# Kernel tuning notes

Hardware: AMD Instinct MI355X
Metric: run time of the kernel (lower is better)

## Reference

```python
import jax, jax.numpy as jnp
import numpy as np

B, S, IN, D, H, FF, L = 16, 1000, 32, 512, 8, 2048, 6
DK = D // H
EPS = 1e-5


def setup_inputs() -> dict:
    key = jax.random.key(0)
    ks = iter(jax.random.split(key, 64))
    def w(shape, s=0.02):
        return jax.random.normal(next(ks), shape, dtype=jnp.float32) * s
    inp = {
        'x': jax.random.normal(next(ks), (B, S, IN), dtype=jnp.float32),
        # input projection
        'Win': w((IN, D)), 'b_in': jnp.zeros((D,), jnp.float32),
        # per-layer attention weights (stacked over L layers)
        'Wq': w((L, D, D)), 'bq': jnp.zeros((L, D), jnp.float32),
        'Wk': w((L, D, D)), 'bk': jnp.zeros((L, D), jnp.float32),
        'Wv': w((L, D, D)), 'bv': jnp.zeros((L, D), jnp.float32),
        'Wo': w((L, D, D)), 'bo': jnp.zeros((L, D), jnp.float32),
        # per-layer feed-forward
        'W1': w((L, D, FF)), 'b1': jnp.zeros((L, FF), jnp.float32),
        'W2': w((L, FF, D)), 'b2': jnp.zeros((L, D), jnp.float32),
        # per-layer layernorms
        'ln1_g': jnp.ones((L, D), jnp.float32), 'ln1_b': jnp.zeros((L, D), jnp.float32),
        'ln2_g': jnp.ones((L, D), jnp.float32), 'ln2_b': jnp.zeros((L, D), jnp.float32),
        # final encoder norm
        'lnf_g': jnp.ones((D,), jnp.float32), 'lnf_b': jnp.zeros((D,), jnp.float32),
        # feature extraction head: D -> D/2 -> D/4
        'Wf1': w((D, D // 2)), 'bf1': jnp.zeros((D // 2,), jnp.float32),
        'Wf2': w((D // 2, D // 4)), 'bf2': jnp.zeros((D // 4,), jnp.float32),
        # reconstruction head: D/4 -> D/2 -> D -> IN
        'Wr1': w((D // 4, D // 2)), 'br1': jnp.zeros((D // 2,), jnp.float32),
        'Wr2': w((D // 2, D)), 'br2': jnp.zeros((D,), jnp.float32),
        'Wr3': w((D, IN)), 'br3': jnp.zeros((IN,), jnp.float32),
        # anomaly head: D/4 -> D/8 -> 1
        'Wa1': w((D // 4, D // 8)), 'ba1': jnp.zeros((D // 8,), jnp.float32),
        'Wa2': w((D // 8, 1)), 'ba2': jnp.zeros((1,), jnp.float32),
    }
    return inp


def _layernorm(x, g, b):
    m = jnp.mean(x, axis=-1, keepdims=True)
    v = jnp.var(x, axis=-1, keepdims=True)
    return (x - m) * jax.lax.rsqrt(v + EPS) * g + b


def _pos_encoding(seq_len, d_model):
    pos = jnp.arange(seq_len, dtype=jnp.float32)[:, None]
    div = jnp.exp(jnp.arange(0, d_model, 2, dtype=jnp.float32) * (-np.log(10000.0) / d_model))
    pe = jnp.zeros((seq_len, d_model), jnp.float32)
    pe = pe.at[:, 0::2].set(jnp.sin(pos * div))
    pe = pe.at[:, 1::2].set(jnp.cos(pos * div))
    return pe


def _encoder(h, Wq, bq, Wk, bk, Wv, bv, Wo, bo, W1, b1, W2, b2,
             ln1_g, ln1_b, ln2_g, ln2_b, lnf_g, lnf_b):
    h = h + _pos_encoding(h.shape[1], D)[None]
    scale = 1.0 / np.sqrt(DK)
    for i in range(L):
        # multi-head self-attention
        q = (h @ Wq[i] + bq[i]).reshape(B, S, H, DK).transpose(0, 2, 1, 3)
        k = (h @ Wk[i] + bk[i]).reshape(B, S, H, DK).transpose(0, 2, 1, 3)
        v = (h @ Wv[i] + bv[i]).reshape(B, S, H, DK).transpose(0, 2, 1, 3)
        scores = jnp.einsum('bhsd,bhtd->bhst', q, k) * scale  # [B,H,S,S]
        attn = jax.nn.softmax(scores, axis=-1)
        ctx = jnp.einsum('bhst,bhtd->bhsd', attn, v)
        ctx = ctx.transpose(0, 2, 1, 3).reshape(B, S, D)
        attn_out = ctx @ Wo[i] + bo[i]
        h = _layernorm(h + attn_out, ln1_g[i], ln1_b[i])
        # feed-forward
        ff = jax.nn.relu(h @ W1[i] + b1[i]) @ W2[i] + b2[i]
        h = _layernorm(h + ff, ln2_g[i], ln2_b[i])
    return _layernorm(h, lnf_g, lnf_b)


def reference(x, Win, b_in, Wq, bq, Wk, bk, Wv, bv, Wo, bo, W1, b1, W2, b2,
              ln1_g, ln1_b, ln2_g, ln2_b, lnf_g, lnf_b,
              Wf1, bf1, Wf2, bf2, Wr1, br1, Wr2, br2, Wr3, br3,
              Wa1, ba1, Wa2, ba2):
    h = x @ Win + b_in  # [B,S,D]
    h = _encoder(h, Wq, bq, Wk, bk, Wv, bv, Wo, bo, W1, b1, W2, b2,
                 ln1_g, ln1_b, ln2_g, ln2_b, lnf_g, lnf_b)
    feat = jax.nn.relu(h @ Wf1 + bf1) @ Wf2 + bf2  # [B,S,D/4]
    recon = jax.nn.relu(jax.nn.relu(feat @ Wr1 + br1) @ Wr2 + br2) @ Wr3 + br3  # [B,S,IN]
    anomaly = jax.nn.sigmoid(jax.nn.relu(feat @ Wa1 + ba1) @ Wa2 + ba2)  # [B,S,1]
    return recon, anomaly
```

## Files before the change

### kernel.cpp

```cpp
#include <hip/hip_runtime.h>
#include <hip/hip_bf16.h>
#include <math.h>

#define B_  16
#define S_  1000
#define IN_ 32
#define D_  512
#define H_  8
#define FF_ 2048
#define L_  6
#define DK_ 64
#define M_  (B_ * S_)
#define SP_ 1024

typedef __bf16 bf16x8 __attribute__((ext_vector_type(8)));
typedef float  floatx4 __attribute__((ext_vector_type(4)));

#define FLAG_RELU 1
#define FLAG_BF16 2
#define FLAG_QKV  4

#define QSCALE 0.18033688011112042f

__global__ __launch_bounds__(256) void gemm_mfma(
    const __bf16* __restrict__ A, const __bf16* __restrict__ BT,
    const float* __restrict__ bias, void* __restrict__ C,
    int M, int N, int K, int flags)
{
    __shared__ __bf16 Asm[2][128 * 32];
    __shared__ __bf16 Bsm[2][128 * 32];

    int tid  = threadIdx.x;
    int wave = tid >> 6;
    int lane = tid & 63;
    int bm = blockIdx.y * 128;
    int bn = blockIdx.x * 128;
    int wm = (wave & 1) * 64;
    int wn = (wave >> 1) * 64;
    int lm = lane & 15;
    int lq = lane >> 4;

    floatx4 acc[4][4] = {};

    int crow  = tid >> 2;
    int cpart = (tid & 3) * 8;
    const __bf16* ag0 = A + (size_t)(bm + crow) * K + cpart;
    const __bf16* ag1 = A + (size_t)(bm + 64 + crow) * K + cpart;
    int nr0 = bn + crow, nr1 = bn + 64 + crow;
    const __bf16* bg0 = BT + (size_t)nr0 * K + cpart;
    const __bf16* bg1 = BT + (size_t)nr1 * K + cpart;
    bool bv0 = nr0 < N, bv1 = nr1 < N;

    uint4 pa0, pa1, pb0, pb1;
    pa0 = *(const uint4*)ag0;
    pa1 = *(const uint4*)ag1;
    pb0 = bv0 ? *(const uint4*)bg0 : make_uint4(0, 0, 0, 0);
    pb1 = bv1 ? *(const uint4*)bg1 : make_uint4(0, 0, 0, 0);

    for (int k0 = 0, it = 0; k0 < K; k0 += 32, ++it) {
        const int cur = it & 1;
        *(uint4*)&Asm[cur][tid * 8]        = pa0;
        *(uint4*)&Asm[cur][2048 + tid * 8] = pa1;
        *(uint4*)&Bsm[cur][tid * 8]        = pb0;
        *(uint4*)&Bsm[cur][2048 + tid * 8] = pb1;
        __syncthreads();

        if (k0 + 32 < K) {
            pa0 = *(const uint4*)(ag0 + k0 + 32);
            pa1 = *(const uint4*)(ag1 + k0 + 32);
            pb0 = bv0 ? *(const uint4*)(bg0 + k0 + 32) : make_uint4(0, 0, 0, 0);
            pb1 = bv1 ? *(const uint4*)(bg1 + k0 + 32) : make_uint4(0, 0, 0, 0);
        }

        bf16x8 af[4], bf[4];
        #pragma unroll
        for (int i = 0; i < 4; ++i) {
            af[i] = *(const bf16x8*)&Asm[cur][(wm + i * 16 + lm) * 32 + lq * 8];
            bf[i] = *(const bf16x8*)&Bsm[cur][(wn + i * 16 + lm) * 32 + lq * 8];
        }
        #pragma unroll
        for (int i = 0; i < 4; ++i)
            #pragma unroll
            for (int j = 0; j < 4; ++j)
                acc[i][j] = __builtin_amdgcn_mfma_f32_16x16x32_bf16(
                    af[i], bf[j], acc[i][j], 0, 0, 0);
    }

    if (flags & FLAG_QKV) {
        int sec = bn >> 9;
        if (sec < 2) {
            __bf16* dst = (__bf16*)C + (sec ? (size_t)8192000 : 0);
            #pragma unroll
            for (int j = 0; j < 4; ++j) {
                int col = (bn & 511) + wn + j * 16 + lm;
                float bvv = bias[bn + wn + j * 16 + lm];
                #pragma unroll
                for (int i = 0; i < 4; ++i)
                    #pragma unroll
                    for (int r = 0; r < 4; ++r) {
                        int m = bm + wm + i * 16 + lq * 4 + r;
                        dst[(size_t)m * 512 + col] = (__bf16)(acc[i][j][r] + bvv);
                    }
            }
        } else {
            __bf16* vt = (__bf16*)C + (size_t)16384000;
            int bbq[4], s0[4];
            #pragma unroll
            for (int i = 0; i < 4; ++i) {
                int m0 = bm + wm + i * 16 + lq * 4;
                bbq[i] = m0 / 1000;
                s0[i]  = m0 - bbq[i] * 1000;
            }
            #pragma unroll
            for (int j = 0; j < 4; ++j) {
                int col = (bn & 511) + wn + j * 16 + lm;
                float bvv = bias[bn + wn + j * 16 + lm];
                int head = col >> 6, dk = col & 63;
                #pragma unroll
                for (int i = 0; i < 4; ++i) {
                    __bf16 t4[4];
                    #pragma unroll
                    for (int r = 0; r < 4; ++r) t4[r] = (__bf16)(acc[i][j][r] + bvv);
                    *(uint2*)(vt + ((size_t)(bbq[i] * H_ + head) * DK_ + dk) * SP_ + s0[i])
                        = *(uint2*)t4;
                }
            }
        }
        return;
    }

    #pragma unroll
    for (int j = 0; j < 4; ++j) {
        int n = bn + wn + j * 16 + lm;
        if (n >= N) continue;
        float bv = bias[n];
        #pragma unroll
        for (int i = 0; i < 4; ++i) {
            #pragma unroll
            for (int r = 0; r < 4; ++r) {
                int m = bm + wm + i * 16 + lq * 4 + r;
                float v = acc[i][j][r] + bv;
                if (flags & FLAG_RELU) v = fmaxf(v, 0.f);
                if (flags & FLAG_BF16) ((__bf16*)C)[(size_t)m * N + n] = (__bf16)v;
                else                   ((float*)C)[(size_t)m * N + n] = v;
            }
        }
    }
}

__device__ __forceinline__ void trans_tile(
    const float* __restrict__ src, __bf16* __restrict__ dst,
    int K, int N, float scale, int tx0, int ty0)
{
    __shared__ float t[32][33];
    int n0 = tx0 * 32, k0 = ty0 * 32;
    int tx = threadIdx.x & 31, ty = threadIdx.x >> 5;
    #pragma unroll
    for (int i = 0; i < 32; i += 8) {
        int k = k0 + ty + i, n = n0 + tx;
        t[ty + i][tx] = (k < K && n < N) ? src[(size_t)k * N + n] * scale : 0.f;
    }
    __syncthreads();
    #pragma unroll
    for (int i = 0; i < 32; i += 8) {
        int n = n0 + ty + i, k = k0 + tx;
        if (n < N && k < K) dst[(size_t)n * K + k] = (__bf16)t[tx][ty + i];
    }
}

__global__ __launch_bounds__(256) void transpose_qkvo(
    const float* __restrict__ Wq, const float* __restrict__ Wk,
    const float* __restrict__ Wv, const float* __restrict__ Wo,
    __bf16* __restrict__ WqkvT, __bf16* __restrict__ WoT)
{
    int l = blockIdx.z >> 2, which = blockIdx.z & 3;
    const float* src; __bf16* dst; float sc = 1.f;
    size_t so = (size_t)l * 512 * 512;
    if (which == 0)      { src = Wq + so; dst = WqkvT + (size_t)l * 1536 * 512; sc = QSCALE; }
    else if (which == 1) { src = Wk + so; dst = WqkvT + (size_t)l * 1536 * 512 + 512 * 512; }
    else if (which == 2) { src = Wv + so; dst = WqkvT + (size_t)l * 1536 * 512 + 1024 * 512; }
    else                 { src = Wo + so; dst = WoT + so; }
    trans_tile(src, dst, 512, 512, sc, blockIdx.x, blockIdx.y);
}

__global__ __launch_bounds__(256) void transpose_ffn(
    const float* __restrict__ W1, const float* __restrict__ W2,
    __bf16* __restrict__ W1T, __bf16* __restrict__ W2T)
{
    int l = blockIdx.z >> 1, which = blockIdx.z & 1;
    size_t so = (size_t)l * 512 * 2048;
    int K = which ? 2048 : 512, N = which ? 512 : 2048;
    if ((int)blockIdx.x >= N / 32 || (int)blockIdx.y >= K / 32) return;
    trans_tile((which ? W2 : W1) + so, (which ? W2T : W1T) + so,
               K, N, 1.f, blockIdx.x, blockIdx.y);
}

struct TDesc { const float* src; __bf16* dst; int K; int N; float scale; };
struct TDescArr { TDesc d[7]; };

__global__ __launch_bounds__(256) void transpose_misc(TDescArr ds)
{
    TDesc t = ds.d[blockIdx.z];
    if ((int)blockIdx.x * 32 >= t.N || (int)blockIdx.y * 32 >= t.K) return;
    trans_tile(t.src, t.dst, t.K, t.N, t.scale, blockIdx.x, blockIdx.y);
}

__global__ void cast_bf16(const float* __restrict__ src, __bf16* __restrict__ dst, int n)
{
    int i = blockIdx.x * 256 + threadIdx.x;
    if (i < n) dst[i] = (__bf16)src[i];
}

__global__ void concat_bias(const float* __restrict__ bq, const float* __restrict__ bk,
                            const float* __restrict__ bv, float* __restrict__ dst)
{
    int i = blockIdx.x * 256 + threadIdx.x;
    if (i >= L_ * 1536) return;
    int l = i / 1536, j = i - l * 1536;
    float v = (j < 512) ? bq[l * 512 + j] * QSCALE
            : (j < 1024) ? bk[l * 512 + j - 512]
                         : bv[l * 512 + j - 1024];
    dst[i] = v;
}

__global__ void add_pos_kernel(float* __restrict__ h, __bf16* __restrict__ hb)
{
    int idx = blockIdx.x * 256 + threadIdx.x;
    if (idx >= B_ * S_ * D_) return;
    int d = idx % D_;
    int s = (idx / D_) % S_;
    int two_i = d & ~1;
    float ang = (float)s * expf((float)two_i * (-9.210340371976184f / (float)D_));
    float v = h[idx] + ((d & 1) ? cosf(ang) : sinf(ang));
    h[idx] = v;
    hb[idx] = (__bf16)v;
}

#define AST 72

__global__ __launch_bounds__(256) void attn_mfma(
    const __bf16* __restrict__ q, const __bf16* __restrict__ k,
    const __bf16* __restrict__ vt, __bf16* __restrict__ ctx)
{
    const int id = blockIdx.x;
    const int w  = (id & 7) * 128 + (id >> 3);
    const int qt = w & 7, hh = (w >> 3) & 7, bb = w >> 6;

    const int tid = threadIdx.x;
    const int wave = tid >> 6, lane = tid & 63;
    const int lm = lane & 15, lq = lane >> 4;

    __shared__ __bf16 Ks[64 * AST];
    __shared__ __bf16 Vt[64 * AST];

    const size_t headbase = (size_t)bb * S_ * D_ + hh * DK_;
    const __bf16* kbase  = k + headbase;
    const __bf16* vtbase = vt + (size_t)(bb * H_ + hh) * DK_ * SP_;

    bf16x8 af[2][2] = {};
    #pragma unroll
    for (int iq = 0; iq < 2; ++iq) {
        int qrow = qt * 128 + wave * 32 + iq * 16 + lm;
        if (qrow < S_) {
            const __bf16* qp = q + headbase + (size_t)qrow * D_;
            af[iq][0] = *(const bf16x8*)(qp + lq * 8);
            af[iq][1] = *(const bf16x8*)(qp + 32 + lq * 8);
        }
    }

    floatx4 oacc[2][4] = {};
    floatx4 lacc[2] = {};

    bf16x8 ones8;
    #pragma unroll
    for (int j = 0; j < 8; ++j) ones8[j] = (__bf16)1.f;

    const int sr  = tid >> 3;
    const int sc8 = (tid & 7) * 8;
    const int colA = (sc8 & 32) | ((sc8 & 8) << 1) | ((sc8 & 16) >> 2);

    uint4 ku[2], vu[2];
    #pragma unroll
    for (int i = 0; i < 2; ++i) {
        int r = sr + i * 32;
        ku[i] = *(const uint4*)(kbase + (size_t)r * D_ + sc8);
        vu[i] = *(const uint4*)(vtbase + (size_t)r * SP_ + sc8);
    }

    for (int jt = 0; jt < 16; ++jt) {
        const int t0 = jt * 64;
        const bool tail = (jt == 15);

        __syncthreads();
        #pragma unroll
        for (int i = 0; i < 2; ++i) {
            int r = sr + i * 32;
            *(uint4*)&Ks[r * AST + sc8] = ku[i];
            uint2 vlo = make_uint2(vu[i].x, vu[i].y);
            uint2 vhi = make_uint2(vu[i].z, vu[i].w);
            *(uint2*)&Vt[r * AST + colA]     = vlo;
            *(uint2*)&Vt[r * AST + colA + 8] = vhi;
        }
        __syncthreads();

        if (jt < 15) {
            int t0n = t0 + 64;
            #pragma unroll
            for (int i = 0; i < 2; ++i) {
                int r = sr + i * 32;
                int trow = t0n + r;
                ku[i] = (trow < S_) ? *(const uint4*)(kbase + (size_t)trow * D_ + sc8)
                                    : make_uint4(0, 0, 0, 0);
                vu[i] = *(const uint4*)(vtbase + (size_t)r * SP_ + t0n + sc8);
            }
        }

        #pragma unroll
        for (int iq = 0; iq < 2; ++iq) {
            floatx4 sacc[4] = {};
            #pragma unroll
            for (int ks = 0; ks < 2; ++ks)
                #pragma unroll
                for (int jb = 0; jb < 4; ++jb) {
                    bf16x8 kf = *(const bf16x8*)&Ks[(jb * 16 + lm) * AST + ks * 32 + lq * 8];
                    sacc[jb] = __builtin_amdgcn_mfma_f32_16x16x32_bf16(
                        kf, af[iq][ks], sacc[jb], 0, 0, 0);
                }

            bf16x8 pf[2];
            if (!tail) {
                #pragma unroll
                for (int jb = 0; jb < 4; ++jb)
                    #pragma unroll
                    for (int r = 0; r < 4; ++r)
                        pf[jb >> 1][(jb & 1) * 4 + r] = (__bf16)exp2f(sacc[jb][r]);
            } else {
                #pragma unroll
                for (int jb = 0; jb < 4; ++jb)
                    #pragma unroll
                    for (int r = 0; r < 4; ++r) {
                        bool valid = (t0 + jb * 16 + lq * 4 + r) < S_;
                        pf[jb >> 1][(jb & 1) * 4 + r] =
                            valid ? (__bf16)exp2f(sacc[jb][r]) : (__bf16)0.f;
                    }
            }

            #pragma unroll
            for (int ks = 0; ks < 2; ++ks) {
                #pragma unroll
                for (int jb = 0; jb < 4; ++jb) {
                    bf16x8 bvf = *(const bf16x8*)&Vt[(jb * 16 + lm) * AST + ks * 32 + lq * 8];
                    oacc[iq][jb] = __builtin_amdgcn_mfma_f32_16x16x32_bf16(
                        pf[ks], bvf, oacc[iq][jb], 0, 0, 0);
                }
                lacc[iq] = __builtin_amdgcn_mfma_f32_16x16x32_bf16(
                    pf[ks], ones8, lacc[iq], 0, 0, 0);
            }
        }
    }

    #pragma unroll
    for (int iq = 0; iq < 2; ++iq) {
        float linv[4];
        #pragma unroll
        for (int r = 0; r < 4; ++r)
            linv[r] = 1.f / lacc[iq][r];
        #pragma unroll
        for (int jb = 0; jb < 4; ++jb)
            #pragma unroll
            for (int r = 0; r < 4; ++r) {
                int srow = qt * 128 + wave * 32 + iq * 16 + lq * 4 + r;
                if (srow < S_)
                    ctx[headbase + (size_t)srow * D_ + jb * 16 + lm] =
                        (__bf16)(oacc[iq][jb][r] * linv[r]);
            }
    }
}

__global__ __launch_bounds__(256) void ln_kernel(
    const float* __restrict__ x, const __bf16* __restrict__ delta,
    const float* __restrict__ g, const float* __restrict__ b,
    float* __restrict__ out, __bf16* __restrict__ outb, int has_delta)
{
    int row = blockIdx.x;
    int tid = threadIdx.x;
    __shared__ float red[256];

    const size_t base = (size_t)row * D_;
    float v0 = x[base + tid];
    float v1 = x[base + tid + 256];
    if (has_delta) {
        v0 += (float)delta[base + tid];
        v1 += (float)delta[base + tid + 256];
    }
    red[tid] = v0 + v1; __syncthreads();
    for (int o = 128; o > 0; o >>= 1) {
        if (tid < o) red[tid] += red[tid + o];
        __syncthreads();
    }
    float mean = red[0] * (1.f / D_);
    __syncthreads();
    float d0 = v0 - mean, d1 = v1 - mean;
    red[tid] = d0 * d0 + d1 * d1; __syncthreads();
    for (int o = 128; o > 0; o >>= 1) {
        if (tid < o) red[tid] += red[tid + o];
        __syncthreads();
    }
    float rstd = rsqrtf(red[0] * (1.f / D_) + 1e-5f);
    float o0 = d0 * rstd * g[tid]       + b[tid];
    float o1 = d1 * rstd * g[tid + 256] + b[tid + 256];
    out[base + tid]        = o0;
    out[base + tid + 256]  = o1;
    outb[base + tid]       = (__bf16)o0;
    outb[base + tid + 256] = (__bf16)o1;
}

__global__ __launch_bounds__(256) void a2_kernel(
    const float* __restrict__ a1, const float* __restrict__ Wa2,
    const float* __restrict__ ba2, float* __restrict__ out)
{
    int row = blockIdx.x * 4 + (threadIdx.x >> 6);
    int lane = threadIdx.x & 63;
    if (row >= M_) return;
    float p = a1[(size_t)row * 64 + lane] * Wa2[lane];
    for (int o = 32; o > 0; o >>= 1) p += __shfl_down(p, o, 64);
    if (lane == 0) out[row] = 1.f / (1.f + expf(-(p + ba2[0])));
}

extern "C" void kernel_launch(void* const* d_in, const int* in_sizes, int n_in,
                              void* d_out, int out_size, void* d_ws, size_t ws_size,
                              hipStream_t stream)
{
    const float* x     = (const float*)d_in[0];
    const float* Win   = (const float*)d_in[1];
    const float* b_in  = (const float*)d_in[2];
    const float* Wq    = (const float*)d_in[3];
    const float* bq    = (const float*)d_in[4];
    const float* Wk    = (const float*)d_in[5];
    const float* bk    = (const float*)d_in[6];
    const float* Wv    = (const float*)d_in[7];
    const float* bv    = (const float*)d_in[8];
    const float* Wo    = (const float*)d_in[9];
    const float* bo    = (const float*)d_in[10];
    const float* W1    = (const float*)d_in[11];
    const float* b1    = (const float*)d_in[12];
    const float* W2    = (const float*)d_in[13];
    const float* b2    = (const float*)d_in[14];
    const float* ln1_g = (const float*)d_in[15];
    const float* ln1_b = (const float*)d_in[16];
    const float* ln2_g = (const float*)d_in[17];
    const float* ln2_b = (const float*)d_in[18];
    const float* lnf_g = (const float*)d_in[19];
    const float* lnf_b = (const float*)d_in[20];
    const float* Wf1   = (const float*)d_in[21];
    const float* bf1   = (const float*)d_in[22];
    const float* Wf2   = (const float*)d_in[23];
    const float* bf2   = (const float*)d_in[24];
    const float* Wr1   = (const float*)d_in[25];
    const float* br1   = (const float*)d_in[26];
    const float* Wr2   = (const float*)d_in[27];
    const float* br2   = (const float*)d_in[28];
    const float* Wr3   = (const float*)d_in[29];
    const float* br3   = (const float*)d_in[30];
    const float* Wa1   = (const float*)d_in[31];
    const float* ba1   = (const float*)d_in[32];
    const float* Wa2   = (const float*)d_in[33];
    const float* ba2   = (const float*)d_in[34];

    float* recon_out   = (float*)d_out;
    float* anomaly_out = (float*)d_out + (size_t)M_ * IN_;

    char* ws = (char*)d_ws;
    float*  h    = (float*)(ws + 0);
    __bf16* tmpb = (__bf16*)(ws + 32768000);
    __bf16* hb   = (__bf16*)(ws + 65536000);
    __bf16* qb   = (__bf16*)(ws + 81920000);
    __bf16* kb   = (__bf16*)(ws + 98304000);
    __bf16* vtb  = (__bf16*)(ws + 114688000);
    __bf16* ctxb = (__bf16*)(ws + 131465216);
    __bf16* ffmid = qb;

    __bf16* t1b   = (__bf16*)(ws + 81920000);
    __bf16* featb = (__bf16*)(ws + 90112000);
    __bf16* r1b   = (__bf16*)(ws + 94208000);
    __bf16* r2b   = (__bf16*)(ws + 102400000);
    float*  a1b   = (float*)(ws + 118784000);

    size_t woff = 147849216;
    auto alloc_bf = [&](size_t elems) { __bf16* p = (__bf16*)(ws + woff); woff += elems * 2; return p; };
    __bf16* WinT  = alloc_bf(32 * 512);
    __bf16* WqkvT = alloc_bf((size_t)L_ * 1536 * 512);
    __bf16* WoT   = alloc_bf((size_t)L_ * 512 * 512);
    __bf16* W1T   = alloc_bf((size_t)L_ * 512 * 2048);
    __bf16* W2T   = alloc_bf((size_t)L_ * 2048 * 512);
    __bf16* Wf1T  = alloc_bf(512 * 256);
    __bf16* Wf2T  = alloc_bf(256 * 128);
    __bf16* Wr1T  = alloc_bf(128 * 256);
    __bf16* Wr2T  = alloc_bf(256 * 512);
    __bf16* Wr3T  = alloc_bf(512 * 32);
    __bf16* Wa1T  = alloc_bf(128 * 64);
    __bf16* xb    = alloc_bf((size_t)M_ * IN_);
    float*  bqkv  = (float*)(ws + woff);  woff += (size_t)L_ * 1536 * 4;

    dim3 blk(256);
    auto gg = [](int N) { return dim3((N + 127) / 128, M_ / 128); };

    hipLaunchKernelGGL(transpose_qkvo, dim3(16, 16, L_ * 4), blk, 0, stream,
                       Wq, Wk, Wv, Wo, WqkvT, WoT);
    hipLaunchKernelGGL(transpose_ffn, dim3(64, 64, L_ * 2), blk, 0, stream,
                       W1, W2, W1T, W2T);
    TDescArr misc;
    misc.d[0] = {Win, WinT, 32, 512, 1.f};
    misc.d[1] = {Wf1, Wf1T, 512, 256, 1.f};
    misc.d[2] = {Wf2, Wf2T, 256, 128, 1.f};
    misc.d[3] = {Wr1, Wr1T, 128, 256, 1.f};
    misc.d[4] = {Wr2, Wr2T, 256, 512, 1.f};
    misc.d[5] = {Wr3, Wr3T, 512, 32, 1.f};
    misc.d[6] = {Wa1, Wa1T, 128, 64, 1.f};
    hipLaunchKernelGGL(transpose_misc, dim3(16, 16, 7), blk, 0, stream, misc);
    hipLaunchKernelGGL(cast_bf16, dim3((M_ * IN_ + 255) / 256), blk, 0, stream,
                       x, xb, M_ * IN_);
    hipLaunchKernelGGL(concat_bias, dim3((L_ * 1536 + 255) / 256), blk, 0, stream,
                       bq, bk, bv, bqkv);

    hipLaunchKernelGGL(gemm_mfma, gg(D_), blk, 0, stream,
                       xb, WinT, b_in, (void*)h, M_, D_, IN_, 0);
    hipLaunchKernelGGL(add_pos_kernel, dim3((B_ * S_ * D_ + 255) / 256), blk, 0, stream,
                       h, hb);

    for (int l = 0; l < L_; ++l) {
        size_t wo = (size_t)l * 512 * 512;
        size_t fo = (size_t)l * 512 * 2048;

        hipLaunchKernelGGL(gemm_mfma, dim3(12, M_ / 128), blk, 0, stream,
                           hb, WqkvT + (size_t)l * 1536 * 512, bqkv + (size_t)l * 1536,
                           (void*)qb, M_, 1536, 512, FLAG_QKV);

        hipLaunchKernelGGL(attn_mfma, dim3(1024), blk, 0, stream,
                           qb, kb, vtb, ctxb);

        hipLaunchKernelGGL(gemm_mfma, gg(D_), blk, 0, stream,
                           ctxb, WoT + wo, bo + (size_t)l * D_, (void*)tmpb, M_, D_, D_,
                           FLAG_BF16);
        hipLaunchKernelGGL(ln_kernel, dim3(M_), blk, 0, stream,
                           h, tmpb, ln1_g + (size_t)l * D_, ln1_b + (size_t)l * D_, h, hb, 1);

        hipLaunchKernelGGL(gemm_mfma, gg(FF_), blk, 0, stream,
                           hb, W1T + fo, b1 + (size_t)l * FF_, (void*)ffmid, M_, FF_, D_,
                           FLAG_RELU | FLAG_BF16);
        hipLaunchKernelGGL(gemm_mfma, gg(D_), blk, 0, stream,
                           ffmid, W2T + fo, b2 + (size_t)l * D_, (void*)tmpb, M_, D_, FF_,
                           FLAG_BF16);
        hipLaunchKernelGGL(ln_kernel, dim3(M_), blk, 0, stream,
                           h, tmpb, ln2_g + (size_t)l * D_, ln2_b + (size_t)l * D_, h, hb, 1);
    }

    hipLaunchKernelGGL(ln_kernel, dim3(M_), blk, 0, stream,
                       h, nullptr, lnf_g, lnf_b, h, hb, 0);

    hipLaunchKernelGGL(gemm_mfma, gg(256), blk, 0, stream,
                       hb, Wf1T, bf1, (void*)t1b, M_, 256, 512, FLAG_RELU | FLAG_BF16);
    hipLaunchKernelGGL(gemm_mfma, gg(128), blk, 0, stream,
                       t1b, Wf2T, bf2, (void*)featb, M_, 128, 256, FLAG_BF16);

    hipLaunchKernelGGL(gemm_mfma, gg(256), blk, 0, stream,
                       featb, Wr1T, br1, (void*)r1b, M_, 256, 128, FLAG_RELU | FLAG_BF16);
    hipLaunchKernelGGL(gemm_mfma, gg(512), blk, 0, stream,
                       r1b, Wr2T, br2, (void*)r2b, M_, 512, 256, FLAG_RELU | FLAG_BF16);
    hipLaunchKernelGGL(gemm_mfma, gg(IN_), blk, 0, stream,
                       r2b, Wr3T, br3, (void*)recon_out, M_, IN_, 512, 0);

    hipLaunchKernelGGL(gemm_mfma, gg(64), blk, 0, stream,
                       featb, Wa1T, ba1, (void*)a1b, M_, 64, 128, FLAG_RELU);
    hipLaunchKernelGGL(a2_kernel, dim3((M_ + 3) / 4), blk, 0, stream,
                       a1b, Wa2, ba2, anomaly_out);
}
```

Before: 1.959 ms.

## Remap GEMM workgroups across XCDs and deepen register prefetch to two stages

Workgroup IDs are remapped so consecutive output tiles land on the same XCD, which should improve L2 reuse of shared A/B panels on the multi-die MI355X. The K loop is also unrolled by two with two register prefetch sets, so global loads run two K-steps ahead of the MFMA work. This adds register pressure, which could reduce occupancy.

```diff
diff --git a/kernel.cpp b/kernel.cpp
--- a/kernel.cpp
+++ b/kernel.cpp
@@ -33,8 +33,15 @@
     int tid  = threadIdx.x;
     int wave = tid >> 6;
     int lane = tid & 63;
-    int bm = blockIdx.y * 128;
-    int bn = blockIdx.x * 128;
+
+    int gx = gridDim.x, nwg = gx * (int)gridDim.y;
+    int orig = blockIdx.y * gx + blockIdx.x;
+    int qq = nwg >> 3, rr = nwg & 7;
+    int xcd = orig & 7, loc = orig >> 3;
+    int nid = (xcd < rr ? xcd * (qq + 1) : rr * (qq + 1) + (xcd - rr) * qq) + loc;
+    int bm = (nid / gx) * 128;
+    int bn = (nid % gx) * 128;
+
     int wm = (wave & 1) * 64;
     int wn = (wave >> 1) * 64;
     int lm = lane & 15;
@@ -51,32 +58,24 @@
     const __bf16* bg1 = BT + (size_t)nr1 * K + cpart;
     bool bv0 = nr0 < N, bv1 = nr1 < N;
 
-    uint4 pa0, pa1, pb0, pb1;
-    pa0 = *(const uint4*)ag0;
-    pa1 = *(const uint4*)ag1;
-    pb0 = bv0 ? *(const uint4*)bg0 : make_uint4(0, 0, 0, 0);
-    pb1 = bv1 ? *(const uint4*)bg1 : make_uint4(0, 0, 0, 0);
-
-    for (int k0 = 0, it = 0; k0 < K; k0 += 32, ++it) {
-        const int cur = it & 1;
-        *(uint4*)&Asm[cur][tid * 8]        = pa0;
-        *(uint4*)&Asm[cur][2048 + tid * 8] = pa1;
-        *(uint4*)&Bsm[cur][tid * 8]        = pb0;
-        *(uint4*)&Bsm[cur][2048 + tid * 8] = pb1;
+    auto kstep = [&](int buf, uint4& ra0, uint4& ra1, uint4& rb0, uint4& rb1,
+                     int knext) {
+        *(uint4*)&Asm[buf][tid * 8]        = ra0;
+        *(uint4*)&Asm[buf][2048 + tid * 8] = ra1;
+        *(uint4*)&Bsm[buf][tid * 8]        = rb0;
+        *(uint4*)&Bsm[buf][2048 + tid * 8] = rb1;
         __syncthreads();
-
-        if (k0 + 32 < K) {
-            pa0 = *(const uint4*)(ag0 + k0 + 32);
-            pa1 = *(const uint4*)(ag1 + k0 + 32);
-            pb0 = bv0 ? *(const uint4*)(bg0 + k0 + 32) : make_uint4(0, 0, 0, 0);
-            pb1 = bv1 ? *(const uint4*)(bg1 + k0 + 32) : make_uint4(0, 0, 0, 0);
-        }
-
+        if (knext < K) {
+            ra0 = *(const uint4*)(ag0 + knext);
+            ra1 = *(const uint4*)(ag1 + knext);
+            rb0 = bv0 ? *(const uint4*)(bg0 + knext) : make_uint4(0, 0, 0, 0);
+            rb1 = bv1 ? *(const uint4*)(bg1 + knext) : make_uint4(0, 0, 0, 0);
+        }
         bf16x8 af[4], bf[4];
         #pragma unroll
         for (int i = 0; i < 4; ++i) {
-            af[i] = *(const bf16x8*)&Asm[cur][(wm + i * 16 + lm) * 32 + lq * 8];
-            bf[i] = *(const bf16x8*)&Bsm[cur][(wn + i * 16 + lm) * 32 + lq * 8];
+            af[i] = *(const bf16x8*)&Asm[buf][(wm + i * 16 + lm) * 32 + lq * 8];
+            bf[i] = *(const bf16x8*)&Bsm[buf][(wn + i * 16 + lm) * 32 + lq * 8];
         }
         #pragma unroll
         for (int i = 0; i < 4; ++i)
@@ -84,6 +83,25 @@
             for (int j = 0; j < 4; ++j)
                 acc[i][j] = __builtin_amdgcn_mfma_f32_16x16x32_bf16(
                     af[i], bf[j], acc[i][j], 0, 0, 0);
+    };
+
+    uint4 a0A, a1A, b0A, b1A;
+    uint4 a0B, a1B, b0B, b1B;
+    a0A = *(const uint4*)ag0;
+    a1A = *(const uint4*)ag1;
+    b0A = bv0 ? *(const uint4*)bg0 : make_uint4(0, 0, 0, 0);
+    b1A = bv1 ? *(const uint4*)bg1 : make_uint4(0, 0, 0, 0);
+    if (32 < K) {
+        a0B = *(const uint4*)(ag0 + 32);
+        a1B = *(const uint4*)(ag1 + 32);
+        b0B = bv0 ? *(const uint4*)(bg0 + 32) : make_uint4(0, 0, 0, 0);
+        b1B = bv1 ? *(const uint4*)(bg1 + 32) : make_uint4(0, 0, 0, 0);
+    }
+
+    for (int k0 = 0; k0 < K; k0 += 64) {
+        kstep(0, a0A, a1A, b0A, b1A, k0 + 64);
+        if (k0 + 32 < K)
+            kstep(1, a0B, a1B, b0B, b1B, k0 + 96);
     }
 
     if (flags & FLAG_QKV) {
```

New measurement: 1.980 ms. No clear change (+1.1%).
